# Kernel tuning notes

Hardware: AMD Instinct MI355X
Metric: run time of the kernel (lower is better)

## Reference

```python
import jax, jax.numpy as jnp
import numpy as np

N, IN_CAPS, IN_LEN = 32, 1152, 32
OUT_CAPS, OUT_LEN = 64, 32
NUM_ITERATIONS = 3


def setup_inputs() -> dict:
    key = jax.random.key(0)
    k1, k2 = jax.random.split(key)
    x = jax.random.normal(k1, (N, IN_CAPS, IN_LEN), dtype=jnp.float32)
    # learnable weight, torch.randn init: (out_capsules, out_length, in_length)
    weight = jax.random.normal(k2, (OUT_CAPS, OUT_LEN, IN_LEN), dtype=jnp.float32)
    return {"x": x, "weight": weight}


def _squash(v):
    # v * ||v|| / (1 + ||v||^2)  ==  (||v||^2/(1+||v||^2)) * v/||v||
    norm_sq = jnp.sum(v * v, axis=-1, keepdims=True)
    norm = jnp.sqrt(norm_sq)
    return v * norm / (1.0 + norm_sq)


def reference(x, weight):
    # priors u_hat: [N, out_caps, in_caps, out_len]
    priors = jnp.einsum('oli,bni->bonl', weight, x)
    logits = jnp.zeros_like(priors)
    output = None
    for r in range(NUM_ITERATIONS):
        # coupling coefficients: softmax over output capsules (axis=1)
        probs = jax.nn.softmax(logits, axis=1)
        # weighted sum over input capsules -> [N, out_caps, 1, out_len]
        output = jnp.sum(probs * priors, axis=-2, keepdims=True)
        if r != NUM_ITERATIONS - 1:
            output = _squash(output)
            # agreement update: [N, out_caps, in_caps, 1]
            logits = logits + jnp.sum(priors * output, axis=-1, keepdims=True)
    output = _squash(output)  # squash=True default
    return jnp.squeeze(output, axis=-2)  # [N, out_caps, out_len]
```

## Files before the change

### kernel.cpp

```cpp
#include <hip/hip_runtime.h>
#include <math.h>


#define N_B      32
#define IN_CAPS  1152
#define IN_LEN   32
#define OUT_CAPS 64
#define OUT_LEN  32

#define NCHUNK 16
#define NPB    (IN_CAPS / NCHUNK)
#define PASS_WAVES 4
#define NPW    (NPB / PASS_WAVES)

__global__ __launch_bounds__(256) void k_init(const float* __restrict__ x,
                                              const float* __restrict__ W,
                                              float* __restrict__ T) {
    const int b   = blockIdx.x;
    const int tid = threadIdx.x;
    const float* xb = x + (size_t)b * IN_CAPS * IN_LEN;

    __shared__ float4 red4[32][8];
    {
        const int q = tid & 7;
        const int g = tid >> 3;
        float4 acc = make_float4(0.f, 0.f, 0.f, 0.f);
        for (int n = g; n < IN_CAPS; n += 32) {
            const float4 v = *(const float4*)(xb + n * IN_LEN + q * 4);
            acc.x += v.x; acc.y += v.y; acc.z += v.z; acc.w += v.w;
        }
        red4[g][q] = acc;
    }
    __syncthreads();
    __shared__ float s0[IN_LEN];
    if (tid < 8) {
        float4 v = make_float4(0.f, 0.f, 0.f, 0.f);
        for (int g = 0; g < 32; ++g) {
            const float4 r = red4[g][tid];
            v.x += r.x; v.y += r.y; v.z += r.z; v.w += r.w;
        }
        const float inv = 1.f / 64.f;
        s0[tid * 4 + 0] = v.x * inv;
        s0[tid * 4 + 1] = v.y * inv;
        s0[tid * 4 + 2] = v.z * inv;
        s0[tid * 4 + 3] = v.w * inv;
    }
    __syncthreads();

    __shared__ float u[OUT_CAPS * OUT_LEN];
    for (int e = tid; e < OUT_CAPS * OUT_LEN; e += 256) {
        const float* wrow = W + (size_t)e * IN_LEN;
        float a = 0.f;
#pragma unroll
        for (int i = 0; i < IN_LEN; ++i) a = fmaf(wrow[i], s0[i], a);
        u[e] = a;
    }
    __syncthreads();

    __shared__ float scale[OUT_CAPS];
    if (tid < OUT_CAPS) {
        float ns = 0.f;
#pragma unroll
        for (int l = 0; l < OUT_LEN; ++l) { const float v = u[tid * OUT_LEN + l]; ns = fmaf(v, v, ns); }
        scale[tid] = sqrtf(ns) / (1.f + ns);
    }
    __syncthreads();

    for (int e = tid; e < OUT_CAPS * IN_LEN; e += 256) {
        const int o = e >> 5, i = e & 31;
        float a = 0.f;
#pragma unroll
        for (int l = 0; l < OUT_LEN; ++l)
            a = fmaf(W[((size_t)o * OUT_LEN + l) * IN_LEN + i], u[o * OUT_LEN + l], a);
        T[(size_t)b * OUT_CAPS * IN_LEN + e] = a * scale[o];
    }
}

__global__ __launch_bounds__(256) void k_pass(const float* __restrict__ x,
                                              const float* __restrict__ T,
                                              float* __restrict__ part) {
    const int b    = blockIdx.x >> 4;
    const int c    = blockIdx.x & (NCHUNK - 1);
    const int lane = threadIdx.x & 63;
    const int wave = __builtin_amdgcn_readfirstlane(threadIdx.x >> 6);

    float t[IN_LEN], s[IN_LEN];
    {
        const float* Trow = T + ((size_t)b * OUT_CAPS + lane) * IN_LEN;
#pragma unroll
        for (int i = 0; i < IN_LEN; ++i) { t[i] = Trow[i]; s[i] = 0.f; }
    }

    const float* xb = x + ((size_t)b * IN_CAPS + c * NPB + wave * NPW) * IN_LEN;
    for (int j = 0; j < NPW; ++j) {
        const float* xn = xb + j * IN_LEN;
        float xv[IN_LEN];
#pragma unroll
        for (int i = 0; i < IN_LEN; ++i) xv[i] = xn[i];

        float logit = 0.f;
#pragma unroll
        for (int i = 0; i < IN_LEN; ++i) logit = fmaf(xv[i], t[i], logit);

        float m = logit;
#pragma unroll
        for (int off = 32; off >= 1; off >>= 1) m = fmaxf(m, __shfl_xor(m, off, 64));
        const float p = __expf(logit - m);
        float sum = p;
#pragma unroll
        for (int off = 32; off >= 1; off >>= 1) sum += __shfl_xor(sum, off, 64);
        const float prob = p / sum;

#pragma unroll
        for (int i = 0; i < IN_LEN; ++i) s[i] = fmaf(prob, xv[i], s[i]);
    }

    __shared__ __align__(16) float sp[PASS_WAVES * OUT_CAPS * IN_LEN];
    {
        float4* dst = (float4*)&sp[(wave * OUT_CAPS + lane) * IN_LEN];
#pragma unroll
        for (int q = 0; q < 8; ++q)
            dst[q] = make_float4(s[4 * q], s[4 * q + 1], s[4 * q + 2], s[4 * q + 3]);
    }
    __syncthreads();
    {
        const float4* sp4 = (const float4*)sp;
        float4* pb4 = (float4*)(part + ((size_t)b * NCHUNK + c) * OUT_CAPS * IN_LEN);
        for (int e = threadIdx.x; e < OUT_CAPS * IN_LEN / 4; e += 256) {
            const float4 a0 = sp4[e];
            const float4 a1 = sp4[512 + e];
            const float4 a2 = sp4[1024 + e];
            const float4 a3 = sp4[1536 + e];
            pb4[e] = make_float4(a0.x + a1.x + a2.x + a3.x,
                                 a0.y + a1.y + a2.y + a3.y,
                                 a0.z + a1.z + a2.z + a3.z,
                                 a0.w + a1.w + a2.w + a3.w);
        }
    }
}

__global__ __launch_bounds__(256) void k_vt(const float* __restrict__ W,
                                            const float* __restrict__ part,
                                            float* __restrict__ T,
                                            float* __restrict__ out,
                                            int final_iter) {
    const int b   = blockIdx.x;
    const int tid = threadIdx.x;

    __shared__ float s_lds[OUT_CAPS * IN_LEN];
    {
        const float4* pb4 = (const float4*)(part + (size_t)b * NCHUNK * OUT_CAPS * IN_LEN);
        for (int e = tid; e < OUT_CAPS * IN_LEN / 4; e += 256) {
            float4 acc = make_float4(0.f, 0.f, 0.f, 0.f);
#pragma unroll
            for (int c = 0; c < NCHUNK; ++c) {
                const float4 v = pb4[c * (OUT_CAPS * IN_LEN / 4) + e];
                acc.x += v.x; acc.y += v.y; acc.z += v.z; acc.w += v.w;
            }
            ((float4*)s_lds)[e] = acc;
        }
    }
    __syncthreads();

    __shared__ float u[OUT_CAPS * OUT_LEN];
    for (int e = tid; e < OUT_CAPS * OUT_LEN; e += 256) {
        const int o = e >> 5;
        const float* wrow = W + (size_t)e * IN_LEN;
        const float* srow = s_lds + o * IN_LEN;
        float a = 0.f;
#pragma unroll
        for (int i = 0; i < IN_LEN; ++i) a = fmaf(wrow[i], srow[i], a);
        u[e] = a;
    }
    __syncthreads();

    __shared__ float scale[OUT_CAPS];
    if (tid < OUT_CAPS) {
        float ns = 0.f;
#pragma unroll
        for (int l = 0; l < OUT_LEN; ++l) { const float v = u[tid * OUT_LEN + l]; ns = fmaf(v, v, ns); }
        scale[tid] = sqrtf(ns) / (1.f + ns);
    }
    __syncthreads();

    if (final_iter) {
        for (int e = tid; e < OUT_CAPS * OUT_LEN; e += 256)
            out[(size_t)b * OUT_CAPS * OUT_LEN + e] = u[e] * scale[e >> 5];
    } else {
        for (int e = tid; e < OUT_CAPS * IN_LEN; e += 256) {
            const int o = e >> 5, i = e & 31;
            float a = 0.f;
#pragma unroll
            for (int l = 0; l < OUT_LEN; ++l)
                a = fmaf(W[((size_t)o * OUT_LEN + l) * IN_LEN + i], u[o * OUT_LEN + l], a);
            T[(size_t)b * OUT_CAPS * IN_LEN + e] += a * scale[o];
        }
    }
}

extern "C" void kernel_launch(void* const* d_in, const int* in_sizes, int n_in,
                              void* d_out, int out_size, void* d_ws, size_t ws_size,
                              hipStream_t stream) {
    const float* x = (const float*)d_in[0];
    const float* W = (const float*)d_in[1];
    float* out = (float*)d_out;

    float* T    = (float*)d_ws;
    float* part = T + (size_t)N_B * OUT_CAPS * IN_LEN;

    k_init<<<N_B, 256, 0, stream>>>(x, W, T);
    k_pass<<<N_B * NCHUNK, 256, 0, stream>>>(x, T, part);
    k_vt  <<<N_B, 256, 0, stream>>>(W, part, T, out, 0);
    k_pass<<<N_B * NCHUNK, 256, 0, stream>>>(x, T, part);
    k_vt  <<<N_B, 256, 0, stream>>>(W, part, T, out, 1);
}
```

Baseline: 140.9 us.

## Fuse routing reduction into pass kernel via last-block atomic counter

Merges the per-batch reduction and squash/T-update kernel into the pass kernel. Each block atomically increments a per-batch counter after a threadfence, and the last of the 16 chunk blocks for a batch sums the partials and computes the update. This removes two kernel launches and their idle gaps. In exchange it adds atomics and fences, and the tail work now runs serially in a single block per batch.

```diff
diff --git a/kernel.cpp b/kernel.cpp
--- a/kernel.cpp
+++ b/kernel.cpp
@@ -15,9 +15,11 @@
 
 __global__ __launch_bounds__(256) void k_init(const float* __restrict__ x,
                                               const float* __restrict__ W,
-                                              float* __restrict__ T) {
+                                              float* __restrict__ T,
+                                              int* __restrict__ cnt) {
     const int b   = blockIdx.x;
     const int tid = threadIdx.x;
+    if (tid == 0) { cnt[b] = 0; cnt[N_B + b] = 0; }
     const float* xb = x + (size_t)b * IN_CAPS * IN_LEN;
 
     __shared__ float4 red4[32][8];
@@ -76,13 +78,18 @@
     }
 }
 
-__global__ __launch_bounds__(256) void k_pass(const float* __restrict__ x,
-                                              const float* __restrict__ T,
-                                              float* __restrict__ part) {
+__global__ __launch_bounds__(256) void k_pass_vt(const float* __restrict__ x,
+                                                 const float* __restrict__ W,
+                                                 float* __restrict__ T,
+                                                 float* __restrict__ part,
+                                                 int* __restrict__ cnt,
+                                                 float* __restrict__ out,
+                                                 int final_iter) {
     const int b    = blockIdx.x >> 4;
     const int c    = blockIdx.x & (NCHUNK - 1);
     const int lane = threadIdx.x & 63;
     const int wave = __builtin_amdgcn_readfirstlane(threadIdx.x >> 6);
+    const int tid  = threadIdx.x;
 
     float t[IN_LEN], s[IN_LEN];
     {
@@ -126,7 +133,7 @@
     {
         const float4* sp4 = (const float4*)sp;
         float4* pb4 = (float4*)(part + ((size_t)b * NCHUNK + c) * OUT_CAPS * IN_LEN);
-        for (int e = threadIdx.x; e < OUT_CAPS * IN_LEN / 4; e += 256) {
+        for (int e = tid; e < OUT_CAPS * IN_LEN / 4; e += 256) {
             const float4 a0 = sp4[e];
             const float4 a1 = sp4[512 + e];
             const float4 a2 = sp4[1024 + e];
@@ -137,24 +144,26 @@
                                  a0.w + a1.w + a2.w + a3.w);
         }
     }
-}
-
-__global__ __launch_bounds__(256) void k_vt(const float* __restrict__ W,
-                                            const float* __restrict__ part,
-                                            float* __restrict__ T,
-                                            float* __restrict__ out,
-                                            int final_iter) {
-    const int b   = blockIdx.x;
-    const int tid = threadIdx.x;
-
-    __shared__ float s_lds[OUT_CAPS * IN_LEN];
+
+    __threadfence();
+    __syncthreads();
+    __shared__ int last_flag;
+    if (tid == 0) last_flag = (atomicAdd(&cnt[b], 1) == NCHUNK - 1);
+    __syncthreads();
+    if (!last_flag) return;
+    __threadfence();
+
+    float* s_lds = sp;
+    float* u     = sp + OUT_CAPS * IN_LEN;
+    float* scale = sp + 2 * OUT_CAPS * IN_LEN;
+
     {
         const float4* pb4 = (const float4*)(part + (size_t)b * NCHUNK * OUT_CAPS * IN_LEN);
         for (int e = tid; e < OUT_CAPS * IN_LEN / 4; e += 256) {
             float4 acc = make_float4(0.f, 0.f, 0.f, 0.f);
 #pragma unroll
-            for (int c = 0; c < NCHUNK; ++c) {
-                const float4 v = pb4[c * (OUT_CAPS * IN_LEN / 4) + e];
+            for (int c2 = 0; c2 < NCHUNK; ++c2) {
+                const float4 v = pb4[c2 * (OUT_CAPS * IN_LEN / 4) + e];
                 acc.x += v.x; acc.y += v.y; acc.z += v.z; acc.w += v.w;
             }
             ((float4*)s_lds)[e] = acc;
@@ -162,7 +171,6 @@
     }
     __syncthreads();
 
-    __shared__ float u[OUT_CAPS * OUT_LEN];
     for (int e = tid; e < OUT_CAPS * OUT_LEN; e += 256) {
         const int o = e >> 5;
         const float* wrow = W + (size_t)e * IN_LEN;
@@ -174,7 +182,6 @@
     }
     __syncthreads();
 
-    __shared__ float scale[OUT_CAPS];
     if (tid < OUT_CAPS) {
         float ns = 0.f;
 #pragma unroll
@@ -207,10 +214,9 @@
 
     float* T    = (float*)d_ws;
     float* part = T + (size_t)N_B * OUT_CAPS * IN_LEN;
-
-    k_init<<<N_B, 256, 0, stream>>>(x, W, T);
-    k_pass<<<N_B * NCHUNK, 256, 0, stream>>>(x, T, part);
-    k_vt  <<<N_B, 256, 0, stream>>>(W, part, T, out, 0);
-    k_pass<<<N_B * NCHUNK, 256, 0, stream>>>(x, T, part);
-    k_vt  <<<N_B, 256, 0, stream>>>(W, part, T, out, 1);
+    int*   cnt  = (int*)(part + (size_t)N_B * NCHUNK * OUT_CAPS * IN_LEN);
+
+    k_init   <<<N_B, 256, 0, stream>>>(x, W, T, cnt);
+    k_pass_vt<<<N_B * NCHUNK, 256, 0, stream>>>(x, W, T, part, cnt,       out, 0);
+    k_pass_vt<<<N_B * NCHUNK, 256, 0, stream>>>(x, W, T, part, cnt + N_B, out, 1);
 }
```

Measured after the change: 271.7 us. 92.9% more time.

## Stage x and T in LDS, batch logits per wave, write per-wave partials

Applied to the files above, without the earlier changes.

k_pass now loads the T tile and the chunk's x rows into LDS once, including a transposed column copy of x. Each wave computes all 18 logits as an outer-product style accumulation, then runs the softmaxes and the weighted sum from LDS. This replaces the serial per-row loop that read x through uncached broadcast global loads. The in-block cross-wave reduction and its barrier are removed; each wave writes its own partial, so k_vt must sum 64 partials instead of 16. That quadruples partial-buffer traffic and workspace use, and raises LDS use per block.

```diff
diff --git a/kernel.cpp b/kernel.cpp
--- a/kernel.cpp
+++ b/kernel.cpp
@@ -12,6 +12,7 @@
 #define NPB    (IN_CAPS / NCHUNK)
 #define PASS_WAVES 4
 #define NPW    (NPB / PASS_WAVES)
+#define NPART  (NCHUNK * PASS_WAVES)
 
 __global__ __launch_bounds__(256) void k_init(const float* __restrict__ x,
                                               const float* __restrict__ W,
@@ -76,66 +77,99 @@
     }
 }
 
-__global__ __launch_bounds__(256) void k_pass(const float* __restrict__ x,
-                                              const float* __restrict__ T,
-                                              float* __restrict__ part) {
+__global__ __launch_bounds__(256, 4) void k_pass(const float* __restrict__ x,
+                                                 const float* __restrict__ T,
+                                                 float* __restrict__ part) {
     const int b    = blockIdx.x >> 4;
     const int c    = blockIdx.x & (NCHUNK - 1);
-    const int lane = threadIdx.x & 63;
-    const int wave = __builtin_amdgcn_readfirstlane(threadIdx.x >> 6);
-
-    float t[IN_LEN], s[IN_LEN];
-    {
-        const float* Trow = T + ((size_t)b * OUT_CAPS + lane) * IN_LEN;
-#pragma unroll
-        for (int i = 0; i < IN_LEN; ++i) { t[i] = Trow[i]; s[i] = 0.f; }
-    }
-
-    const float* xb = x + ((size_t)b * IN_CAPS + c * NPB + wave * NPW) * IN_LEN;
-    for (int j = 0; j < NPW; ++j) {
-        const float* xn = xb + j * IN_LEN;
-        float xv[IN_LEN];
-#pragma unroll
-        for (int i = 0; i < IN_LEN; ++i) xv[i] = xn[i];
-
-        float logit = 0.f;
-#pragma unroll
-        for (int i = 0; i < IN_LEN; ++i) logit = fmaf(xv[i], t[i], logit);
-
-        float m = logit;
+    const int tid  = threadIdx.x;
+    const int lane = tid & 63;
+    const int wave = __builtin_amdgcn_readfirstlane(tid >> 6);
+
+    __shared__ float T_lds[OUT_CAPS * 33];
+    __shared__ __align__(16) float x_row[NPB * IN_LEN];
+    __shared__ __align__(16) float x_col[IN_LEN * 80];
+
+    {
+        const float4* T4 = (const float4*)(T + (size_t)b * OUT_CAPS * IN_LEN);
+        for (int e = tid; e < OUT_CAPS * IN_LEN / 4; e += 256) {
+            const float4 v = T4[e];
+            const int o = e >> 3, q = e & 7;
+            float* d = &T_lds[o * 33 + q * 4];
+            d[0] = v.x; d[1] = v.y; d[2] = v.z; d[3] = v.w;
+        }
+    }
+    {
+        const float4* X4 = (const float4*)(x + ((size_t)b * IN_CAPS + c * NPB) * IN_LEN);
+        for (int e = tid; e < NPB * IN_LEN / 4; e += 256) {
+            const float4 v = X4[e];
+            ((float4*)x_row)[e] = v;
+            const int n = e >> 3, q = e & 7;
+            const int wq = n / NPW, idx = n - wq * NPW;
+            float* d = &x_col[(q * 4) * 80 + wq * 20 + idx];
+            d[0] = v.x; d[80] = v.y; d[160] = v.z; d[240] = v.w;
+        }
+    }
+    __syncthreads();
+
+    float acc[NPW];
+#pragma unroll
+    for (int n = 0; n < NPW; ++n) acc[n] = 0.f;
+
+#define FMA4A(v, k0) \
+    acc[k0+0] = fmaf(tv, (v).x, acc[k0+0]); \
+    acc[k0+1] = fmaf(tv, (v).y, acc[k0+1]); \
+    acc[k0+2] = fmaf(tv, (v).z, acc[k0+2]); \
+    acc[k0+3] = fmaf(tv, (v).w, acc[k0+3]);
+
+#pragma unroll
+    for (int i = 0; i < IN_LEN; ++i) {
+        const float tv = T_lds[lane * 33 + i];
+        const float4* xr = (const float4*)&x_col[i * 80 + wave * 20];
+        const float4 a0 = xr[0], a1 = xr[1], a2 = xr[2], a3 = xr[3], a4 = xr[4];
+        FMA4A(a0, 0) FMA4A(a1, 4) FMA4A(a2, 8) FMA4A(a3, 12)
+        acc[16] = fmaf(tv, a4.x, acc[16]);
+        acc[17] = fmaf(tv, a4.y, acc[17]);
+    }
+#undef FMA4A
+
+    float prob[NPW];
+#pragma unroll
+    for (int n = 0; n < NPW; ++n) {
+        float m = acc[n];
 #pragma unroll
         for (int off = 32; off >= 1; off >>= 1) m = fmaxf(m, __shfl_xor(m, off, 64));
-        const float p = __expf(logit - m);
-        float sum = p;
-#pragma unroll
-        for (int off = 32; off >= 1; off >>= 1) sum += __shfl_xor(sum, off, 64);
-        const float prob = p / sum;
-
-#pragma unroll
-        for (int i = 0; i < IN_LEN; ++i) s[i] = fmaf(prob, xv[i], s[i]);
-    }
-
-    __shared__ __align__(16) float sp[PASS_WAVES * OUT_CAPS * IN_LEN];
-    {
-        float4* dst = (float4*)&sp[(wave * OUT_CAPS + lane) * IN_LEN];
+        const float p = __expf(acc[n] - m);
+        float ssum = p;
+#pragma unroll
+        for (int off = 32; off >= 1; off >>= 1) ssum += __shfl_xor(ssum, off, 64);
+        prob[n] = p / ssum;
+    }
+
+    float s[IN_LEN];
+#pragma unroll
+    for (int i = 0; i < IN_LEN; ++i) s[i] = 0.f;
+
+#pragma unroll
+    for (int n = 0; n < NPW; ++n) {
+        const float pn = prob[n];
+        const float4* xr = (const float4*)&x_row[(wave * NPW + n) * IN_LEN];
+#pragma unroll
+        for (int q = 0; q < 8; ++q) {
+            const float4 v = xr[q];
+            s[q * 4 + 0] = fmaf(pn, v.x, s[q * 4 + 0]);
+            s[q * 4 + 1] = fmaf(pn, v.y, s[q * 4 + 1]);
+            s[q * 4 + 2] = fmaf(pn, v.z, s[q * 4 + 2]);
+            s[q * 4 + 3] = fmaf(pn, v.w, s[q * 4 + 3]);
+        }
+    }
+
+    {
+        float4* dst = (float4*)(part +
+            ((((size_t)b * NCHUNK + c) * PASS_WAVES + wave) * OUT_CAPS + lane) * IN_LEN);
 #pragma unroll
         for (int q = 0; q < 8; ++q)
             dst[q] = make_float4(s[4 * q], s[4 * q + 1], s[4 * q + 2], s[4 * q + 3]);
-    }
-    __syncthreads();
-    {
-        const float4* sp4 = (const float4*)sp;
-        float4* pb4 = (float4*)(part + ((size_t)b * NCHUNK + c) * OUT_CAPS * IN_LEN);
-        for (int e = threadIdx.x; e < OUT_CAPS * IN_LEN / 4; e += 256) {
-            const float4 a0 = sp4[e];
-            const float4 a1 = sp4[512 + e];
-            const float4 a2 = sp4[1024 + e];
-            const float4 a3 = sp4[1536 + e];
-            pb4[e] = make_float4(a0.x + a1.x + a2.x + a3.x,
-                                 a0.y + a1.y + a2.y + a3.y,
-                                 a0.z + a1.z + a2.z + a3.z,
-                                 a0.w + a1.w + a2.w + a3.w);
-        }
     }
 }
 
@@ -149,11 +183,11 @@
 
     __shared__ float s_lds[OUT_CAPS * IN_LEN];
     {
-        const float4* pb4 = (const float4*)(part + (size_t)b * NCHUNK * OUT_CAPS * IN_LEN);
+        const float4* pb4 = (const float4*)(part + (size_t)b * NPART * OUT_CAPS * IN_LEN);
         for (int e = tid; e < OUT_CAPS * IN_LEN / 4; e += 256) {
             float4 acc = make_float4(0.f, 0.f, 0.f, 0.f);
-#pragma unroll
-            for (int c = 0; c < NCHUNK; ++c) {
+#pragma unroll 8
+            for (int c = 0; c < NPART; ++c) {
                 const float4 v = pb4[c * (OUT_CAPS * IN_LEN / 4) + e];
                 acc.x += v.x; acc.y += v.y; acc.z += v.z; acc.w += v.w;
             }
```

New measurement: 164.7 us. 17.0% more time.

## Optimize routing pass inner loop with DPP reductions, vector loads, padded LDS

Applied to the files above, without the earlier changes.

Rewrites the k_pass inner loop to load x rows as float4, split the dot product into four independent accumulators, and fully unroll over input capsules. Wave max/sum reductions now use DPP row operations for the first four stages instead of shuffles, and division is replaced by a fast reciprocal. The LDS staging buffer is padded to 36 floats per row to avoid bank conflicts, and launch bounds request two blocks per CU. Full unrolling of 72 iterations may bloat code size and register pressure.

```diff
diff --git a/kernel.cpp b/kernel.cpp
--- a/kernel.cpp
+++ b/kernel.cpp
@@ -12,6 +12,28 @@
 #define NPB    (IN_CAPS / NCHUNK)
 #define PASS_WAVES 4
 #define NPW    (NPB / PASS_WAVES)
+
+#define DPPV(v, ctrl) \
+    __int_as_float(__builtin_amdgcn_update_dpp(0, __float_as_int(v), ctrl, 0xF, 0xF, true))
+
+__device__ __forceinline__ float wave_max(float v) {
+    v = fmaxf(v, DPPV(v, 0xB1));
+    v = fmaxf(v, DPPV(v, 0x4E));
+    v = fmaxf(v, DPPV(v, 0x141));
+    v = fmaxf(v, DPPV(v, 0x140));
+    v = fmaxf(v, __shfl_xor(v, 16, 64));
+    v = fmaxf(v, __shfl_xor(v, 32, 64));
+    return v;
+}
+__device__ __forceinline__ float wave_sum(float v) {
+    v += DPPV(v, 0xB1);
+    v += DPPV(v, 0x4E);
+    v += DPPV(v, 0x141);
+    v += DPPV(v, 0x140);
+    v += __shfl_xor(v, 16, 64);
+    v += __shfl_xor(v, 32, 64);
+    return v;
+}
 
 __global__ __launch_bounds__(256) void k_init(const float* __restrict__ x,
                                               const float* __restrict__ W,
@@ -76,61 +98,84 @@
     }
 }
 
-__global__ __launch_bounds__(256) void k_pass(const float* __restrict__ x,
-                                              const float* __restrict__ T,
-                                              float* __restrict__ part) {
+__global__ __launch_bounds__(256, 2) void k_pass(const float* __restrict__ x,
+                                                 const float* __restrict__ T,
+                                                 float* __restrict__ part) {
     const int b    = blockIdx.x >> 4;
     const int c    = blockIdx.x & (NCHUNK - 1);
-    const int lane = threadIdx.x & 63;
-    const int wave = __builtin_amdgcn_readfirstlane(threadIdx.x >> 6);
-
-    float t[IN_LEN], s[IN_LEN];
-    {
-        const float* Trow = T + ((size_t)b * OUT_CAPS + lane) * IN_LEN;
-#pragma unroll
-        for (int i = 0; i < IN_LEN; ++i) { t[i] = Trow[i]; s[i] = 0.f; }
-    }
-
-    const float* xb = x + ((size_t)b * IN_CAPS + c * NPB + wave * NPW) * IN_LEN;
+    const int tid  = threadIdx.x;
+    const int lane = tid & 63;
+    const int wave = __builtin_amdgcn_readfirstlane(tid >> 6);
+
+    float t[IN_LEN];
+    {
+        const float4* Trow4 = (const float4*)(T + ((size_t)b * OUT_CAPS + lane) * IN_LEN);
+#pragma unroll
+        for (int q = 0; q < 8; ++q) {
+            const float4 v = Trow4[q];
+            t[4 * q] = v.x; t[4 * q + 1] = v.y; t[4 * q + 2] = v.z; t[4 * q + 3] = v.w;
+        }
+    }
+    asm volatile("" : "+v"(t[0]), "+v"(t[1]), "+v"(t[2]), "+v"(t[3]),
+                      "+v"(t[4]), "+v"(t[5]), "+v"(t[6]), "+v"(t[7]),
+                      "+v"(t[8]), "+v"(t[9]), "+v"(t[10]), "+v"(t[11]),
+                      "+v"(t[12]), "+v"(t[13]), "+v"(t[14]), "+v"(t[15]));
+    asm volatile("" : "+v"(t[16]), "+v"(t[17]), "+v"(t[18]), "+v"(t[19]),
+                      "+v"(t[20]), "+v"(t[21]), "+v"(t[22]), "+v"(t[23]),
+                      "+v"(t[24]), "+v"(t[25]), "+v"(t[26]), "+v"(t[27]),
+                      "+v"(t[28]), "+v"(t[29]), "+v"(t[30]), "+v"(t[31]));
+
+    float s[IN_LEN];
+#pragma unroll
+    for (int i = 0; i < IN_LEN; ++i) s[i] = 0.f;
+
+    const float* xw = x + ((size_t)b * IN_CAPS + c * NPB + wave * NPW) * IN_LEN;
+
+#define L4(acc, R, k) \
+    acc = fmaf((R).x, t[k],     acc); acc = fmaf((R).y, t[k + 1], acc); \
+    acc = fmaf((R).z, t[k + 2], acc); acc = fmaf((R).w, t[k + 3], acc);
+#define S4(R, k) \
+    s[k]     = fmaf(prob, (R).x, s[k]);     s[k + 1] = fmaf(prob, (R).y, s[k + 1]); \
+    s[k + 2] = fmaf(prob, (R).z, s[k + 2]); s[k + 3] = fmaf(prob, (R).w, s[k + 3]);
+
+#pragma unroll
     for (int j = 0; j < NPW; ++j) {
-        const float* xn = xb + j * IN_LEN;
-        float xv[IN_LEN];
-#pragma unroll
-        for (int i = 0; i < IN_LEN; ++i) xv[i] = xn[i];
-
-        float logit = 0.f;
-#pragma unroll
-        for (int i = 0; i < IN_LEN; ++i) logit = fmaf(xv[i], t[i], logit);
-
-        float m = logit;
-#pragma unroll
-        for (int off = 32; off >= 1; off >>= 1) m = fmaxf(m, __shfl_xor(m, off, 64));
+        const float4* xr = (const float4*)(xw + j * IN_LEN);
+        const float4 r0 = xr[0], r1 = xr[1], r2 = xr[2], r3 = xr[3],
+                     r4 = xr[4], r5 = xr[5], r6 = xr[6], r7 = xr[7];
+
+        float l0 = 0.f, l1 = 0.f, l2 = 0.f, l3 = 0.f;
+        L4(l0, r0, 0)  L4(l1, r1, 4)  L4(l2, r2, 8)  L4(l3, r3, 12)
+        L4(l0, r4, 16) L4(l1, r5, 20) L4(l2, r6, 24) L4(l3, r7, 28)
+        const float logit = (l0 + l1) + (l2 + l3);
+
+        const float m = wave_max(logit);
         const float p = __expf(logit - m);
-        float sum = p;
-#pragma unroll
-        for (int off = 32; off >= 1; off >>= 1) sum += __shfl_xor(sum, off, 64);
-        const float prob = p / sum;
-
-#pragma unroll
-        for (int i = 0; i < IN_LEN; ++i) s[i] = fmaf(prob, xv[i], s[i]);
-    }
-
-    __shared__ __align__(16) float sp[PASS_WAVES * OUT_CAPS * IN_LEN];
-    {
-        float4* dst = (float4*)&sp[(wave * OUT_CAPS + lane) * IN_LEN];
+        const float S = wave_sum(p);
+        const float prob = p * __builtin_amdgcn_rcpf(S);
+
+        S4(r0, 0)  S4(r1, 4)  S4(r2, 8)  S4(r3, 12)
+        S4(r4, 16) S4(r5, 20) S4(r6, 24) S4(r7, 28)
+    }
+#undef L4
+#undef S4
+
+    __shared__ __align__(16) float sp[PASS_WAVES][OUT_CAPS][36];
+    {
+        float4* dst = (float4*)&sp[wave][lane][0];
 #pragma unroll
         for (int q = 0; q < 8; ++q)
             dst[q] = make_float4(s[4 * q], s[4 * q + 1], s[4 * q + 2], s[4 * q + 3]);
     }
     __syncthreads();
     {
-        const float4* sp4 = (const float4*)sp;
         float4* pb4 = (float4*)(part + ((size_t)b * NCHUNK + c) * OUT_CAPS * IN_LEN);
-        for (int e = threadIdx.x; e < OUT_CAPS * IN_LEN / 4; e += 256) {
-            const float4 a0 = sp4[e];
-            const float4 a1 = sp4[512 + e];
-            const float4 a2 = sp4[1024 + e];
-            const float4 a3 = sp4[1536 + e];
+        for (int e = tid; e < OUT_CAPS * IN_LEN / 4; e += 256) {
+            const int o = e >> 3, q4 = (e & 7) * 4;
+            const float4 a0 = *(const float4*)&sp[0][o][q4];
+            const float4 a1 = *(const float4*)&sp[1][o][q4];
+            const float4 a2 = *(const float4*)&sp[2][o][q4];
+            const float4 a3 = *(const float4*)&sp[3][o][q4];
             pb4[e] = make_float4(a0.x + a1.x + a2.x + a3.x,
                                  a0.y + a1.y + a2.y + a3.y,
                                  a0.z + a1.z + a2.z + a3.z,
```

Result: faster. 131.6 us (-6.6%).
